# Performance work log

Measured on AMD Instinct MI355X. Metric: run time of the kernel, lower is better.

The kernel has to match this reference:

```python
import jax, jax.numpy as jnp
import numpy as np

N, E, FT_IN, HID, FT_OUT, H = 32768, 524288, 256, 256, 512, 4
C = HID // H  # per-head dim = 64


def gatv2_conv(x, edge_index, w_l, b_l, w_r, b_r, att, bias):
    """PyG GATv2Conv (eval mode, add_self_loops=True, concat=True)."""
    n = x.shape[0]
    loop = jnp.arange(n)
    src = jnp.concatenate([edge_index[0], loop])  # j (source / neighbor)
    dst = jnp.concatenate([edge_index[1], loop])  # i (target)
    x_l = (x @ w_l + b_l).reshape(n, H, C)
    x_r = (x @ w_r + b_r).reshape(n, H, C)
    e = jax.nn.leaky_relu(x_l[src] + x_r[dst], 0.2)        # [E+N, H, C]
    logits = jnp.einsum('ehc,hc->eh', e, att)              # [E+N, H]
    m = jax.ops.segment_max(logits, dst, num_segments=n)
    m = jnp.where(jnp.isfinite(m), m, 0.0)
    p = jnp.exp(logits - m[dst])
    s = jax.ops.segment_sum(p, dst, num_segments=n)
    alpha = p / (s[dst] + 1e-16)                           # scatter-softmax over in-edges
    out = jax.ops.segment_sum(alpha[:, :, None] * x_l[src], dst, num_segments=n)
    return out.reshape(n, H * C) + bias


def gelu(x):
    return jax.nn.gelu(x, approximate=False)  # torch nn.GELU default (erf)


def setup_inputs() -> dict:
    key = jax.random.key(0)
    ks = jax.random.split(key, 24)
    sc = lambda fan_in: 1.0 / np.sqrt(fan_in)
    d = {
        'x': jax.random.normal(ks[0], (N, FT_IN), jnp.float32),
        'edge_index': jax.random.randint(ks[1], (2, E), 0, N, dtype=jnp.int32),
        'batch': jnp.repeat(jnp.arange(64, dtype=jnp.int32), N // 64),
        'batch_size': 64,
        # conv1 params
        'w1_l': jax.random.normal(ks[2], (FT_IN, HID), jnp.float32) * sc(FT_IN),
        'b1_l': jnp.zeros((HID,), jnp.float32),
        'w1_r': jax.random.normal(ks[3], (FT_IN, HID), jnp.float32) * sc(FT_IN),
        'b1_r': jnp.zeros((HID,), jnp.float32),
        'att1': jax.random.normal(ks[4], (H, C), jnp.float32) * sc(C),
        'bias1': jnp.zeros((HID,), jnp.float32),
        # conv2 params
        'w2_l': jax.random.normal(ks[5], (HID, HID), jnp.float32) * sc(HID),
        'b2_l': jnp.zeros((HID,), jnp.float32),
        'w2_r': jax.random.normal(ks[6], (HID, HID), jnp.float32) * sc(HID),
        'b2_r': jnp.zeros((HID,), jnp.float32),
        'att2': jax.random.normal(ks[7], (H, C), jnp.float32) * sc(C),
        'bias2': jnp.zeros((HID,), jnp.float32),
        # MLP head
        'lin1_w': jax.random.normal(ks[8], (HID, 4 * HID), jnp.float32) * sc(HID),
        'lin1_b': jnp.zeros((4 * HID,), jnp.float32),
        'lin2_w': jax.random.normal(ks[9], (4 * HID, HID), jnp.float32) * sc(4 * HID),
        'lin2_b': jnp.zeros((HID,), jnp.float32),
        'fin_w': jax.random.normal(ks[10], (HID, FT_OUT), jnp.float32) * sc(HID),
        'fin_b': jnp.zeros((FT_OUT,), jnp.float32),
    }
    return d


def reference(x, edge_index, batch, batch_size,
              w1_l, b1_l, w1_r, b1_r, att1, bias1,
              w2_l, b2_l, w2_r, b2_r, att2, bias2,
              lin1_w, lin1_b, lin2_w, lin2_b, fin_w, fin_b):
    h = gatv2_conv(x, edge_index, w1_l, b1_l, w1_r, b1_r, att1, bias1)
    h = gelu(h)
    h = gatv2_conv(h, edge_index, w2_l, b2_l, w2_r, b2_r, att2, bias2)
    # global mean pool per graph
    n_graphs = batch_size
    sums = jax.ops.segment_sum(h, batch, num_segments=n_graphs)
    cnts = jax.ops.segment_sum(jnp.ones((h.shape[0],), h.dtype), batch, num_segments=n_graphs)
    graph_mean = sums / jnp.maximum(cnts, 1.0)[:, None]
    # take node 0 of each graph (dropouts are identity in eval)
    z = h.reshape(batch_size, -1, HID)[:, 0, :]
    z = gelu(z @ lin1_w + lin1_b) @ lin2_w + lin2_b
    z = z @ fin_w + fin_b
    return z, graph_mean
```

## Files before the change

kernel.cpp:

```cpp
#include <hip/hip_runtime.h>
#include <hip/hip_bf16.h>
#include <stdint.h>

typedef __attribute__((ext_vector_type(8))) short short8;
typedef __attribute__((ext_vector_type(4))) short short4v;
typedef __attribute__((ext_vector_type(4))) float floatx4;
typedef __attribute__((ext_vector_type(2))) float floatx2;
typedef __hip_bfloat16 bf16;

__device__ __forceinline__ float b2f(bf16 v) { return __bfloat162float(v); }
__device__ __forceinline__ bf16 f2b(float v) { return __float2bfloat16(v); }
__device__ __forceinline__ float gelu_f(float v) {
    return 0.5f * v * (1.0f + erff(v * 0.70710678118654752f));
}
__device__ __forceinline__ floatx2 cvt2(unsigned v) {
    floatx2 r;
    r.x = __uint_as_float(v << 16);
    r.y = __uint_as_float(v & 0xffff0000u);
    return r;
}

#define GLD_LDS16(gptr, lptr) \
  __builtin_amdgcn_global_load_lds((const __attribute__((address_space(1))) void*)(gptr), \
                                   (__attribute__((address_space(3))) void*)(lptr), 16, 0, 0)


__global__ void k_count_tr(const int* __restrict__ dst, int* __restrict__ cnt, int E,
                           const float* __restrict__ Wl1, const float* __restrict__ Wr1,
                           const float* __restrict__ Wl2, const float* __restrict__ Wr2,
                           bf16* __restrict__ Wt,
                           const float* __restrict__ x, bf16* __restrict__ xb) {
    int bx = blockIdx.x;
    if (bx < 512) {
        int g = bx * 256 + threadIdx.x;
        if (g * 4 < E) {
            int4 d = ((const int4*)dst)[g];
            atomicAdd(&cnt[d.x], 1);
            atomicAdd(&cnt[d.y], 1);
            atomicAdd(&cnt[d.z], 1);
            atomicAdd(&cnt[d.w], 1);
        }
    } else if (bx < 1536) {
        int b = bx - 512;
        int r = b & 255, half = (b >> 8) & 1, layer = b >> 9;
        int c = threadIdx.x;
        const float* W = layer ? (half ? Wr2 : Wl2) : (half ? Wr1 : Wl1);
        Wt[(size_t)(layer * 512 + half * 256 + c) * 256 + r] = f2b(W[r * 256 + c]);
    } else {
        int b = bx - 1536;
        size_t base = ((size_t)b * 256 + threadIdx.x) * 32;
        const float4* xin = (const float4*)(x + base);
        #pragma unroll
        for (int q = 0; q < 4; q++) {
            float4 a = xin[2 * q];
            float4 c = xin[2 * q + 1];
            bf16 t[8] = {f2b(a.x), f2b(a.y), f2b(a.z), f2b(a.w),
                         f2b(c.x), f2b(c.y), f2b(c.z), f2b(c.w)};
            *(short8*)(xb + base + q * 8) = *(const short8*)t;
        }
    }
}

__global__ __launch_bounds__(1024) void k_scan(const int* __restrict__ cnt,
                                               int* __restrict__ row_ptr,
                                               int* __restrict__ fill, int n) {
    __shared__ int sdata[1024];
    int t = threadIdx.x;
    int base = t * 32;
    int local[32];
    const int4* c4 = (const int4*)(cnt + base);
    int vals[32];
    #pragma unroll
    for (int q = 0; q < 8; q++) {
        int4 v = c4[q];
        vals[q * 4 + 0] = v.x; vals[q * 4 + 1] = v.y;
        vals[q * 4 + 2] = v.z; vals[q * 4 + 3] = v.w;
    }
    int sum = 0;
    #pragma unroll
    for (int k = 0; k < 32; k++) { local[k] = sum; sum += vals[k]; }
    sdata[t] = sum;
    __syncthreads();
    for (int off = 1; off < 1024; off <<= 1) {
        int v = (t >= off) ? sdata[t - off] : 0;
        __syncthreads();
        sdata[t] += v;
        __syncthreads();
    }
    int excl = sdata[t] - sum;
    #pragma unroll
    for (int k = 0; k < 32; k++) {
        int v = excl + local[k];
        row_ptr[base + k] = v;
        fill[base + k] = v;
    }
    if (t == 1023) row_ptr[n] = excl + sum;
}

__device__ __forceinline__ void gemm_body(const bf16* __restrict__ A,
                                          const bf16* __restrict__ Bt,
                                          const float* __restrict__ biasL,
                                          const float* __restrict__ biasR,
                                          bf16* __restrict__ C,
                                          int K, int m0, int n0,
                                          bf16* __restrict__ smem) {
    bf16* As = smem;
    bf16* Bs = smem + 8192;
    const int tid  = threadIdx.x;
    const int wave = tid >> 6;
    const int lane = tid & 63;
    const int quad = lane >> 4;
    const int l16  = lane & 15;
    const int wm = (wave & 1) * 64;
    const int wn = (wave >> 1) * 64;
    const int scole = ((lane & 7) ^ (lane >> 3)) * 8;
    const int srow  = lane >> 3;

    floatx4 acc[4][4] = {};

    for (int k0 = 0; k0 < K; k0 += 64) {
        #pragma unroll
        for (int i = 0; i < 4; i++) {
            int chunk = i * 4 + wave;
            int row = chunk * 8 + srow;
            GLD_LDS16(A + (size_t)(m0 + row) * K + k0 + scole,
                      (char*)As + chunk * 1024 + lane * 16);
            GLD_LDS16(Bt + (size_t)(n0 + row) * K + k0 + scole,
                      (char*)Bs + chunk * 1024 + lane * 16);
        }
        __syncthreads();
        #pragma unroll
        for (int ks = 0; ks < 2; ks++) {
            short8 af[4], bfr[4];
            int pk = ((ks * 4 + quad) ^ (l16 & 7)) * 8;
            #pragma unroll
            for (int i = 0; i < 4; i++) {
                af[i]  = *(const short8*)&As[(wm + i * 16 + l16) * 64 + pk];
                bfr[i] = *(const short8*)&Bs[(wn + i * 16 + l16) * 64 + pk];
            }
            #pragma unroll
            for (int i = 0; i < 4; i++)
                #pragma unroll
                for (int j = 0; j < 4; j++)
                    acc[i][j] = __builtin_amdgcn_mfma_f32_16x16x32_bf16(af[i], bfr[j], acc[i][j], 0, 0, 0);
        }
        __syncthreads();
    }

    float bvj[4];
    #pragma unroll
    for (int j = 0; j < 4; j++) {
        int gcol = n0 + wn + j * 16 + l16;
        bvj[j] = (gcol < 256) ? biasL[gcol] : biasR[gcol - 256];
    }
    #pragma unroll
    for (int h = 0; h < 2; h++) {
        if ((wave & 1) == h) {
            #pragma unroll
            for (int j = 0; j < 4; j++) {
                int lcol = wn + j * 16 + l16;
                #pragma unroll
                for (int i = 0; i < 4; i++)
                    #pragma unroll
                    for (int r = 0; r < 4; r++)
                        smem[(i * 16 + quad * 4 + r) * 136 + lcol] = f2b(acc[i][j][r] + bvj[j]);
            }
        }
        __syncthreads();
        {
            int rl = tid >> 4;
            int cs = (tid & 15) * 8;
            #pragma unroll
            for (int p = 0; p < 4; p++) {
                int row = p * 16 + rl;
                short8 v = *(const short8*)&smem[row * 136 + cs];
                *(short8*)(C + (size_t)(m0 + h * 64 + row) * 512 + n0 + cs) = v;
            }
        }
        if (h == 0) __syncthreads();
    }
}

__global__ __launch_bounds__(256) void k_scatter_gemm(const int* __restrict__ src,
                                                      const int* __restrict__ dst,
                                                      int* __restrict__ fill,
                                                      int* __restrict__ col, int E,
                                                      const bf16* __restrict__ A,
                                                      const bf16* __restrict__ Bt,
                                                      const float* __restrict__ biasL,
                                                      const float* __restrict__ biasR,
                                                      bf16* __restrict__ C, int K) {
    __shared__ bf16 smem[16384];
    int bx = blockIdx.x;
    int rem = bx % 3;
    if (rem == 2) {
        int g = (bx / 3) * 256 + threadIdx.x;
        if (g * 4 < E) {
            int4 d = ((const int4*)dst)[g];
            int4 sv = ((const int4*)src)[g];
            int p;
            p = atomicAdd(&fill[d.x], 1); col[p] = sv.x;
            p = atomicAdd(&fill[d.y], 1); col[p] = sv.y;
            p = atomicAdd(&fill[d.z], 1); col[p] = sv.z;
            p = atomicAdd(&fill[d.w], 1); col[p] = sv.w;
        }
    } else {
        int gid = (bx / 3) * 2 + rem;
        int n0 = (gid & 3) * 128;
        int m0 = (gid >> 2) * 128;
        gemm_body(A, Bt, biasL, biasR, C, K, m0, n0, smem);
    }
}

__global__ __launch_bounds__(256) void k_gemm2(const bf16* __restrict__ A,
                                               const bf16* __restrict__ Bt,
                                               const float* __restrict__ biasL,
                                               const float* __restrict__ biasR,
                                               bf16* __restrict__ C, int K) {
    __shared__ bf16 smem[16384];
    int n0 = blockIdx.x * 128;
    int m0 = blockIdx.y * 128;
    gemm_body(A, Bt, biasL, biasR, C, K, m0, n0, smem);
}

__global__ __launch_bounds__(256) void k_agg(const bf16* __restrict__ xlr,
                                             const float* __restrict__ att,
                                             const int* __restrict__ row_ptr,
                                             const int* __restrict__ col,
                                             const float* __restrict__ bias,
                                             bf16* __restrict__ out, int do_gelu) {
    int wave = threadIdx.x >> 6, lane = threadIdx.x & 63;
    int i = blockIdx.x * 4 + wave;
    int hl = lane & 31;
    int half = lane >> 5;
    unsigned f = (hl >> 3) * 64 + (hl & 7) * 8;

    floatx2 att6v[4], att4v[4], xrv[4];
    {
        floatx4 a0 = *(const floatx4*)(att + f);
        floatx4 a1 = *(const floatx4*)(att + f + 4);
        att6v[0] = (floatx2){0.6f * a0[0], 0.6f * a0[1]};
        att6v[1] = (floatx2){0.6f * a0[2], 0.6f * a0[3]};
        att6v[2] = (floatx2){0.6f * a1[0], 0.6f * a1[1]};
        att6v[3] = (floatx2){0.6f * a1[2], 0.6f * a1[3]};
        att4v[0] = (floatx2){0.4f * a0[0], 0.4f * a0[1]};
        att4v[1] = (floatx2){0.4f * a0[2], 0.4f * a0[3]};
        att4v[2] = (floatx2){0.4f * a1[0], 0.4f * a1[1]};
        att4v[3] = (floatx2){0.4f * a1[2], 0.4f * a1[3]};
        unsigned raw[4];
        *(uint4*)raw = *(const uint4*)(xlr + ((unsigned)i * 512u + 256u + f));
        #pragma unroll
        for (int k = 0; k < 4; k++) xrv[k] = cvt2(raw[k]);
    }

    int e0 = row_ptr[i], e1 = row_ptr[i + 1];
    int total = 1 + (e1 - e0);

    int src_c = i;
    if (half == 1 && total > 1) src_c = col[e0];
    unsigned g_cur[4];
    *(uint4*)g_cur = *(const uint4*)(xlr + ((unsigned)src_c * 512u + f));
    int t1 = 2 + half;
    int src_n = (t1 < total) ? col[e0 + t1 - 1] : i;

    float s = 0.f;
    floatx2 acc2[4] = {};

    for (int base = 0; base < total; base += 2) {
        unsigned g_nxt[4];
        *(uint4*)g_nxt = *(const uint4*)(xlr + ((unsigned)src_n * 512u + f));
        int t2 = base + 4 + half;
        int src_n2 = (t2 < total) ? col[e0 + t2 - 1] : i;
        bool valid = (base + half) < total;
        floatx2 xv[4], l2 = {0.f, 0.f};
        #pragma unroll
        for (int k = 0; k < 4; k++) {
            xv[k] = cvt2(g_cur[k]);
            floatx2 u = xv[k] + xrv[k];
            floatx2 au = __builtin_elementwise_abs(u);
            l2 += u * att6v[k];
            l2 += au * att4v[k];
        }
        float l = l2.x + l2.y;
        l += __shfl_xor(l, 1, 8);
        l += __shfl_xor(l, 2, 8);
        l += __shfl_xor(l, 4, 8);
        float p = valid ? __expf(l) : 0.f;
        s += p;
        floatx2 p2 = {p, p};
        #pragma unroll
        for (int k = 0; k < 4; k++) acc2[k] += p2 * xv[k];
        #pragma unroll
        for (int k = 0; k < 4; k++) g_cur[k] = g_nxt[k];
        src_n = src_n2;
    }

    s += __shfl_xor(s, 32, 64);
    #pragma unroll
    for (int k = 0; k < 4; k++) {
        acc2[k].x += __shfl_xor(acc2[k].x, 32, 64);
        acc2[k].y += __shfl_xor(acc2[k].y, 32, 64);
    }

    if (half == 0) {
        float inv = 1.0f / (s + 1e-16f);
        bf16 ov[8];
        #pragma unroll
        for (int k = 0; k < 4; k++) {
            float v0 = acc2[k].x * inv + bias[f + 2 * k];
            float v1 = acc2[k].y * inv + bias[f + 2 * k + 1];
            if (do_gelu) { v0 = gelu_f(v0); v1 = gelu_f(v1); }
            ov[2 * k]     = f2b(v0);
            ov[2 * k + 1] = f2b(v1);
        }
        *(short8*)(out + ((unsigned)i * 256u + f)) = *(const short8*)ov;
    }
}

__device__ __forceinline__ void head_body(const bf16* __restrict__ inB,
                                          const float* __restrict__ inF,
                                          const float* __restrict__ W,
                                          const float* __restrict__ bias,
                                          float* __restrict__ out,
                                          int K, int N, long long row_stride, int act,
                                          int g, int chunk, float* zin, float* red) {
    int t = threadIdx.x;
    int nc = t & 63;
    int kq = t >> 6;
    int n = chunk * 64 + nc;
    for (int k = t; k < K; k += 256)
        zin[k] = inB ? b2f(inB[(size_t)g * row_stride + k])
                     : inF[(size_t)g * row_stride + k];
    __syncthreads();
    const int klen = K >> 2;
    const int kb = kq * klen;
    float acc = 0.f;
    #pragma unroll 8
    for (int k = 0; k < klen; k++)
        acc = fmaf(zin[kb + k], W[(size_t)(kb + k) * N + n], acc);
    red[t] = acc;
    __syncthreads();
    if (kq == 0) {
        float v = red[nc] + red[nc + 64] + red[nc + 128] + red[nc + 192] + bias[n];
        if (act) v = gelu_f(v);
        out[(size_t)g * N + n] = v;
    }
}

__global__ __launch_bounds__(256) void k_pe1(const bf16* __restrict__ hb,
                                             float* __restrict__ part,
                                             const float* __restrict__ lin1w,
                                             const float* __restrict__ lin1b,
                                             float* __restrict__ t1, int PG) {
    __shared__ float zin[256];
    __shared__ float red[256];
    int bx = blockIdx.x;
    if (bx < 512) {
        int g = bx >> 3, p = bx & 7, c = threadIdx.x;
        int rows_per = PG / 8;
        const bf16* base = hb + ((size_t)g * PG + (size_t)p * rows_per) * 256;
        float acc = 0.f;
        for (int r = 0; r < rows_per; r++) acc += b2f(base[(size_t)r * 256 + c]);
        part[((size_t)g * 8 + p) * 256 + c] = acc;
    } else {
        int b = bx - 512;
        head_body(hb, nullptr, lin1w, lin1b, t1, 256, 1024,
                  (long long)PG * 256, 1, b >> 4, b & 15, zin, red);
    }
}

__global__ __launch_bounds__(256) void k_pe2(const float* __restrict__ part,
                                             float* __restrict__ outPool, int PG,
                                             const float* __restrict__ t1,
                                             const float* __restrict__ lin2w,
                                             const float* __restrict__ lin2b,
                                             float* __restrict__ t2) {
    __shared__ float zin[1024];
    __shared__ float red[256];
    int bx = blockIdx.x;
    if (bx < 64) {
        int g = bx, c = threadIdx.x;
        float acc = 0.f;
        for (int p = 0; p < 8; p++) acc += part[((size_t)g * 8 + p) * 256 + c];
        outPool[g * 256 + c] = acc / (float)PG;
    } else {
        int b = bx - 64;
        head_body(nullptr, t1, lin2w, lin2b, t2, 1024, 256,
                  1024, 0, b >> 2, b & 3, zin, red);
    }
}

__global__ __launch_bounds__(256) void k_fin(const float* __restrict__ t2,
                                             const float* __restrict__ finw,
                                             const float* __restrict__ finb,
                                             float* __restrict__ out) {
    __shared__ float zin[256];
    __shared__ float red[256];
    head_body(nullptr, t2, finw, finb, out, 256, 512,
              256, 0, blockIdx.x, blockIdx.y, zin, red);
}

extern "C" void kernel_launch(void* const* d_in, const int* in_sizes, int n_in,
                              void* d_out, int out_size, void* d_ws, size_t ws_size,
                              hipStream_t stream) {
    const float* x     = (const float*)d_in[0];
    const int*   ei    = (const int*)d_in[1];
    const float* w1_l  = (const float*)d_in[4];
    const float* b1_l  = (const float*)d_in[5];
    const float* w1_r  = (const float*)d_in[6];
    const float* b1_r  = (const float*)d_in[7];
    const float* att1  = (const float*)d_in[8];
    const float* bias1 = (const float*)d_in[9];
    const float* w2_l  = (const float*)d_in[10];
    const float* b2_l  = (const float*)d_in[11];
    const float* w2_r  = (const float*)d_in[12];
    const float* b2_r  = (const float*)d_in[13];
    const float* att2  = (const float*)d_in[14];
    const float* bias2 = (const float*)d_in[15];
    const float* lin1w = (const float*)d_in[16];
    const float* lin1b = (const float*)d_in[17];
    const float* lin2w = (const float*)d_in[18];
    const float* lin2b = (const float*)d_in[19];
    const float* finw  = (const float*)d_in[20];
    const float* finb  = (const float*)d_in[21];

    const int N  = in_sizes[0] / 256;
    const int E  = in_sizes[1] / 2;
    const int NG = 64;
    const int PG = N / NG;

    char* ws = (char*)d_ws;
    size_t off = 0;
    bf16* xlr = (bf16*)(ws + off); off += (size_t)N * 512 * 2;
    bf16* hb  = (bf16*)(ws + off); off += (size_t)N * 256 * 2;
    bf16* wt  = (bf16*)(ws + off); off += 2 * 512 * 256 * 2;
    int* row_ptr = (int*)(ws + off); off += (size_t)(N + 4) * 4;
    int* cnt     = (int*)(ws + off); off += (size_t)N * 4;
    int* fill    = (int*)(ws + off); off += (size_t)N * 4;
    int* col     = (int*)(ws + off); off += (size_t)E * 4;
    float* pws   = (float*)(ws + off); off += (size_t)NG * 8 * 256 * 4;
    float* t1    = (float*)(ws + off); off += (size_t)NG * 1024 * 4;
    float* t2    = (float*)(ws + off); off += (size_t)NG * 256 * 4;

    bf16* xb = hb;

    const int* srcv = ei;
    const int* dstv = ei + E;

    hipMemsetAsync(cnt, 0, (size_t)N * 4, stream);
    k_count_tr<<<512 + 1024 + 1024, 256, 0, stream>>>(dstv, cnt, E,
                                                      w1_l, w1_r, w2_l, w2_r, wt, x, xb);
    k_scan<<<1, 1024, 0, stream>>>(cnt, row_ptr, fill, N);

    k_scatter_gemm<<<512 + 1024, 256, 0, stream>>>(srcv, dstv, fill, col, E,
                                                   xb, wt, b1_l, b1_r, xlr, 256);
    k_agg<<<N / 4, 256, 0, stream>>>(xlr, att1, row_ptr, col, bias1, hb, 1);

    dim3 gg(4, N / 128);
    k_gemm2<<<gg, 256, 0, stream>>>(hb, wt + 512 * 256, b2_l, b2_r, xlr, 256);
    k_agg<<<N / 4, 256, 0, stream>>>(xlr, att2, row_ptr, col, bias2, hb, 0);

    float* outp = (float*)d_out;
    k_pe1<<<512 + 1024, 256, 0, stream>>>(hb, pws, lin1w, lin1b, t1, PG);
    k_pe2<<<64 + 256, 256, 0, stream>>>(pws, outp + 64 * 512, PG, t1, lin2w, lin2b, t2);
    dim3 gf(NG, 512 / 64);
    k_fin<<<gf, 256, 0, stream>>>(t2, finw, finb, outp);
}
```

Baseline: 337.2 us.

## Use persistent atomic work-stealing waves in GATv2 aggregation with DPP reductions

The aggregation kernel changes from one wave per node with a fixed grid to a persistent grid of 2048 blocks. Each wave takes its next node index from a global atomic counter, which the scan kernel resets. The goal is to balance the uneven in-degree work and cut block launch overhead. The 8-lane logit reduction now uses DPP adds instead of shuffles, and the logit accumulation is split into two chains. The cost is one atomic per node and possible contention on the counter.

```diff
diff --git a/kernel.cpp b/kernel.cpp
--- a/kernel.cpp
+++ b/kernel.cpp
@@ -18,6 +18,11 @@
     r.x = __uint_as_float(v << 16);
     r.y = __uint_as_float(v & 0xffff0000u);
     return r;
+}
+template <int CTRL>
+__device__ __forceinline__ float dpp_add(float v) {
+    int x = __builtin_amdgcn_update_dpp(0, __float_as_int(v), CTRL, 0xf, 0xf, true);
+    return v + __int_as_float(x);
 }
 
 #define GLD_LDS16(gptr, lptr) \
@@ -63,7 +68,8 @@
 
 __global__ __launch_bounds__(1024) void k_scan(const int* __restrict__ cnt,
                                                int* __restrict__ row_ptr,
-                                               int* __restrict__ fill, int n) {
+                                               int* __restrict__ fill, int n,
+                                               int* __restrict__ ctr) {
     __shared__ int sdata[1024];
     int t = threadIdx.x;
     int base = t * 32;
@@ -94,7 +100,11 @@
         row_ptr[base + k] = v;
         fill[base + k] = v;
     }
-    if (t == 1023) row_ptr[n] = excl + sum;
+    if (t == 1023) {
+        row_ptr[n] = excl + sum;
+        ctr[0] = 0;
+        ctr[1] = 0;
+    }
 }
 
 __device__ __forceinline__ void gemm_body(const bf16* __restrict__ A,
@@ -228,14 +238,14 @@
                                              const int* __restrict__ row_ptr,
                                              const int* __restrict__ col,
                                              const float* __restrict__ bias,
-                                             bf16* __restrict__ out, int do_gelu) {
-    int wave = threadIdx.x >> 6, lane = threadIdx.x & 63;
-    int i = blockIdx.x * 4 + wave;
+                                             bf16* __restrict__ out, int do_gelu,
+                                             int* __restrict__ ctr, int Nn) {
+    int lane = threadIdx.x & 63;
     int hl = lane & 31;
     int half = lane >> 5;
     unsigned f = (hl >> 3) * 64 + (hl & 7) * 8;
 
-    floatx2 att6v[4], att4v[4], xrv[4];
+    floatx2 att6v[4], att4v[4];
     {
         floatx4 a0 = *(const floatx4*)(att + f);
         floatx4 a1 = *(const floatx4*)(att + f + 4);
@@ -247,73 +257,84 @@
         att4v[1] = (floatx2){0.4f * a0[2], 0.4f * a0[3]};
         att4v[2] = (floatx2){0.4f * a1[0], 0.4f * a1[1]};
         att4v[3] = (floatx2){0.4f * a1[2], 0.4f * a1[3]};
-        unsigned raw[4];
-        *(uint4*)raw = *(const uint4*)(xlr + ((unsigned)i * 512u + 256u + f));
-        #pragma unroll
-        for (int k = 0; k < 4; k++) xrv[k] = cvt2(raw[k]);
-    }
-
-    int e0 = row_ptr[i], e1 = row_ptr[i + 1];
-    int total = 1 + (e1 - e0);
-
-    int src_c = i;
-    if (half == 1 && total > 1) src_c = col[e0];
-    unsigned g_cur[4];
-    *(uint4*)g_cur = *(const uint4*)(xlr + ((unsigned)src_c * 512u + f));
-    int t1 = 2 + half;
-    int src_n = (t1 < total) ? col[e0 + t1 - 1] : i;
-
-    float s = 0.f;
-    floatx2 acc2[4] = {};
-
-    for (int base = 0; base < total; base += 2) {
-        unsigned g_nxt[4];
-        *(uint4*)g_nxt = *(const uint4*)(xlr + ((unsigned)src_n * 512u + f));
-        int t2 = base + 4 + half;
-        int src_n2 = (t2 < total) ? col[e0 + t2 - 1] : i;
-        bool valid = (base + half) < total;
-        floatx2 xv[4], l2 = {0.f, 0.f};
+    }
+
+    while (true) {
+        int vtk = 0;
+        if (lane == 0) vtk = atomicAdd(ctr, 1);
+        int i = __builtin_amdgcn_readfirstlane(vtk);
+        if (i >= Nn) break;
+
+        floatx2 xrv[4];
+        {
+            unsigned raw[4];
+            *(uint4*)raw = *(const uint4*)(xlr + ((unsigned)i * 512u + 256u + f));
+            #pragma unroll
+            for (int k = 0; k < 4; k++) xrv[k] = cvt2(raw[k]);
+        }
+
+        int e0 = row_ptr[i], e1 = row_ptr[i + 1];
+        int total = 1 + (e1 - e0);
+
+        int src_c = i;
+        if (half == 1 && total > 1) src_c = col[e0];
+        unsigned g_cur[4];
+        *(uint4*)g_cur = *(const uint4*)(xlr + ((unsigned)src_c * 512u + f));
+        int t1 = 2 + half;
+        int src_n = (t1 < total) ? col[e0 + t1 - 1] : i;
+
+        float s = 0.f;
+        floatx2 acc2[4] = {};
+
+        for (int base = 0; base < total; base += 2) {
+            unsigned g_nxt[4];
+            *(uint4*)g_nxt = *(const uint4*)(xlr + ((unsigned)src_n * 512u + f));
+            int t2 = base + 4 + half;
+            int src_n2 = (t2 < total) ? col[e0 + t2 - 1] : i;
+            bool valid = (base + half) < total;
+            floatx2 xv[4], l2a = {0.f, 0.f}, l2b = {0.f, 0.f};
+            #pragma unroll
+            for (int k = 0; k < 4; k++) {
+                xv[k] = cvt2(g_cur[k]);
+                floatx2 u = xv[k] + xrv[k];
+                floatx2 au = __builtin_elementwise_abs(u);
+                l2a += u * att6v[k];
+                l2b += au * att4v[k];
+            }
+            float l = (l2a.x + l2b.x) + (l2a.y + l2b.y);
+            l = dpp_add<0xB1>(l);
+            l = dpp_add<0x4E>(l);
+            l = dpp_add<0x141>(l);
+            float p = valid ? __expf(l) : 0.f;
+            s += p;
+            floatx2 p2 = {p, p};
+            #pragma unroll
+            for (int k = 0; k < 4; k++) acc2[k] += p2 * xv[k];
+            #pragma unroll
+            for (int k = 0; k < 4; k++) g_cur[k] = g_nxt[k];
+            src_n = src_n2;
+        }
+
+        s += __shfl_xor(s, 32, 64);
         #pragma unroll
         for (int k = 0; k < 4; k++) {
-            xv[k] = cvt2(g_cur[k]);
-            floatx2 u = xv[k] + xrv[k];
-            floatx2 au = __builtin_elementwise_abs(u);
-            l2 += u * att6v[k];
-            l2 += au * att4v[k];
-        }
-        float l = l2.x + l2.y;
-        l += __shfl_xor(l, 1, 8);
-        l += __shfl_xor(l, 2, 8);
-        l += __shfl_xor(l, 4, 8);
-        float p = valid ? __expf(l) : 0.f;
-        s += p;
-        floatx2 p2 = {p, p};
-        #pragma unroll
-        for (int k = 0; k < 4; k++) acc2[k] += p2 * xv[k];
-        #pragma unroll
-        for (int k = 0; k < 4; k++) g_cur[k] = g_nxt[k];
-        src_n = src_n2;
-    }
-
-    s += __shfl_xor(s, 32, 64);
-    #pragma unroll
-    for (int k = 0; k < 4; k++) {
-        acc2[k].x += __shfl_xor(acc2[k].x, 32, 64);
-        acc2[k].y += __shfl_xor(acc2[k].y, 32, 64);
-    }
-
-    if (half == 0) {
-        float inv = 1.0f / (s + 1e-16f);
-        bf16 ov[8];
-        #pragma unroll
-        for (int k = 0; k < 4; k++) {
-            float v0 = acc2[k].x * inv + bias[f + 2 * k];
-            float v1 = acc2[k].y * inv + bias[f + 2 * k + 1];
-            if (do_gelu) { v0 = gelu_f(v0); v1 = gelu_f(v1); }
-            ov[2 * k]     = f2b(v0);
-            ov[2 * k + 1] = f2b(v1);
-        }
-        *(short8*)(out + ((unsigned)i * 256u + f)) = *(const short8*)ov;
+            acc2[k].x += __shfl_xor(acc2[k].x, 32, 64);
+            acc2[k].y += __shfl_xor(acc2[k].y, 32, 64);
+        }
+
+        if (half == 0) {
+            float inv = 1.0f / (s + 1e-16f);
+            bf16 ov[8];
+            #pragma unroll
+            for (int k = 0; k < 4; k++) {
+                float v0 = acc2[k].x * inv + bias[f + 2 * k];
+                float v1 = acc2[k].y * inv + bias[f + 2 * k + 1];
+                if (do_gelu) { v0 = gelu_f(v0); v1 = gelu_f(v1); }
+                ov[2 * k]     = f2b(v0);
+                ov[2 * k + 1] = f2b(v1);
+            }
+            *(short8*)(out + ((unsigned)i * 256u + f)) = *(const short8*)ov;
+        }
     }
 }
 
@@ -441,6 +462,7 @@
     float* pws   = (float*)(ws + off); off += (size_t)NG * 8 * 256 * 4;
     float* t1    = (float*)(ws + off); off += (size_t)NG * 1024 * 4;
     float* t2    = (float*)(ws + off); off += (size_t)NG * 256 * 4;
+    int* ctr     = (int*)(ws + off); off += 16;
 
     bf16* xb = hb;
 
@@ -450,15 +472,15 @@
     hipMemsetAsync(cnt, 0, (size_t)N * 4, stream);
     k_count_tr<<<512 + 1024 + 1024, 256, 0, stream>>>(dstv, cnt, E,
                                                       w1_l, w1_r, w2_l, w2_r, wt, x, xb);
-    k_scan<<<1, 1024, 0, stream>>>(cnt, row_ptr, fill, N);
+    k_scan<<<1, 1024, 0, stream>>>(cnt, row_ptr, fill, N, ctr);
 
     k_scatter_gemm<<<512 + 1024, 256, 0, stream>>>(srcv, dstv, fill, col, E,
                                                    xb, wt, b1_l, b1_r, xlr, 256);
-    k_agg<<<N / 4, 256, 0, stream>>>(xlr, att1, row_ptr, col, bias1, hb, 1);
+    k_agg<<<2048, 256, 0, stream>>>(xlr, att1, row_ptr, col, bias1, hb, 1, ctr, N);
 
     dim3 gg(4, N / 128);
     k_gemm2<<<gg, 256, 0, stream>>>(hb, wt + 512 * 256, b2_l, b2_r, xlr, 256);
-    k_agg<<<N / 4, 256, 0, stream>>>(xlr, att2, row_ptr, col, bias2, hb, 0);
+    k_agg<<<2048, 256, 0, stream>>>(xlr, att2, row_ptr, col, bias2, hb, 0, ctr + 1, N);
 
     float* outp = (float*)d_out;
     k_pe1<<<512 + 1024, 256, 0, stream>>>(hb, pws, lin1w, lin1b, t1, PG);
```

Result: slower. 1.190 ms (+252.8%).
